# Kernel optimization log

Hardware: AMD Instinct MI355X
Metric: run time of the kernel (lower is better)

Reference implementation:

```python
import jax, jax.numpy as jnp
import numpy as np

B, T, D, H = 64, 512, 256, 512  # batch, seq_len, embed_dim, enc_units


def _lstm(x_tbd, U, xW, reverse):
    """Keras LSTM with activation='sigmoid' (all gates AND candidate/output use sigmoid).
    x_tbd: [T,B,D] (only for shape), xW: precomputed x@W+b [T,B,4H], U: [H,4H].
    Gate order in Keras kernels: i, f, c(g), o."""
    if reverse:
        xW = xW[::-1]
    b = xW.shape[1]
    h0 = jnp.zeros((b, U.shape[0]), xW.dtype)
    c0 = jnp.zeros((b, U.shape[0]), xW.dtype)

    def step(carry, xw):
        h, c = carry
        z = xw + h @ U  # [B,4H]
        i, f, g, o = jnp.split(z, 4, axis=-1)
        i = jax.nn.sigmoid(i)
        f = jax.nn.sigmoid(f)
        g = jax.nn.sigmoid(g)  # activation='sigmoid' (not tanh)
        o = jax.nn.sigmoid(o)
        c_new = f * c + i * g
        h_new = o * jax.nn.sigmoid(c_new)  # activation='sigmoid' (not tanh)
        return (h_new, c_new), h_new

    (h_last, c_last), hs = jax.lax.scan(step, (h0, c0), xW)
    if reverse:
        hs = hs[::-1]  # Bidirectional re-reverses backward outputs to align in time
    return hs, h_last, c_last


def setup_inputs() -> dict:
    key = jax.random.key(0)
    ks = jax.random.split(key, 6)
    s_in = 1.0 / np.sqrt(D)
    s_rec = 1.0 / np.sqrt(H)
    return {
        "x": jax.random.normal(ks[0], (B, T, D), jnp.float32),
        "hidden": jax.random.normal(ks[1], (2 * B, H), jnp.float32),  # unused by call()
        "Wf": jax.random.normal(ks[2], (D, 4 * H), jnp.float32) * s_in,
        "Uf": jax.random.normal(ks[3], (H, 4 * H), jnp.float32) * s_rec,
        "bf": jnp.zeros((4 * H,), jnp.float32),
        "Wb": jax.random.normal(ks[4], (D, 4 * H), jnp.float32) * s_in,
        "Ub": jax.random.normal(ks[5], (H, 4 * H), jnp.float32) * s_rec,
        "bb": jnp.zeros((4 * H,), jnp.float32),
    }


def reference(x, hidden, Wf, Uf, bf, Wb, Ub, bb):
    x_tbd = jnp.transpose(x, (1, 0, 2))  # [T,B,D]
    # Precompute input projections for all timesteps (hoisted out of the scan)
    xWf = jnp.einsum('tbd,dh->tbh', x_tbd, Wf) + bf
    xWb = jnp.einsum('tbd,dh->tbh', x_tbd, Wb) + bb
    hs_f, hF, cF = _lstm(x_tbd, Uf, xWf, reverse=False)
    hs_b, hB, cB = _lstm(x_tbd, Ub, xWb, reverse=True)
    out = 0.5 * (hs_f + hs_b)  # merge_mode='ave'
    out = jnp.transpose(out, (1, 0, 2))  # [B,T,H]
    return out, hF, cF, hB, cB
```

## Files before the change

### kernel.cpp

```cpp
#include <hip/hip_runtime.h>
#include <hip/hip_bf16.h>
#include <cstdint>
#include <cstddef>

#define BB 64
#define TT 512
#define DD 256
#define HH 512
#define G4 2048

typedef __bf16 bf16x8 __attribute__((ext_vector_type(8)));
typedef __bf16 bf16x4 __attribute__((ext_vector_type(4)));
typedef float  f32x4  __attribute__((ext_vector_type(4)));
typedef unsigned long long u64;

__device__ __forceinline__ float sigf(float x) {
  return 1.0f / (1.0f + __expf(-x));
}

__device__ __forceinline__ void drain_vmem() {
  asm volatile("s_waitcnt vmcnt(0)" ::: "memory");
}

__global__ void cvt_x_kernel(const float* __restrict__ x, __bf16* __restrict__ xb) {
  int i = (blockIdx.x * 256 + threadIdx.x) * 4;
  float4 v = *(const float4*)(x + i);
  bf16x4 o;
  o[0] = (__bf16)v.x; o[1] = (__bf16)v.y; o[2] = (__bf16)v.z; o[3] = (__bf16)v.w;
  *(bf16x4*)(xb + i) = o;
}

__launch_bounds__(256, 1)
__global__ void lstm_kernel(const __bf16* __restrict__ xb,
                            const float* __restrict__ Wf, const float* __restrict__ Uf,
                            const float* __restrict__ bf_,
                            const float* __restrict__ Wb, const float* __restrict__ Ub,
                            const float* __restrict__ bb_,
                            __bf16* __restrict__ hbuf,
                            unsigned int* __restrict__ flags,
                            float* __restrict__ out,
                            __bf16* __restrict__ hsb) {
  const int bx  = blockIdx.x;
  const int dir = bx >> 5;
  const int s   = bx & 31;
  const float* Wd = dir ? Wb : Wf;
  const float* Ud = dir ? Ub : Uf;
  const float* bd = dir ? bb_ : bf_;
  unsigned int* flbase = flags + (size_t)dir * 32 * 32;
  unsigned int* myflag = flbase + (size_t)s * 32;
  __bf16* hb = hbuf + (size_t)dir * 2 * BB * HH;

  const int tid  = threadIdx.x;
  const int mt   = tid >> 6;
  const int lane = tid & 63;
  const int j    = lane & 15;
  const int q    = lane >> 4;
  const int colg = s * 16 + j;

  bf16x8 wfrag[4][24];
#pragma unroll
  for (int g = 0; g < 4; ++g) {
    const int col = g * HH + colg;
#pragma unroll
    for (int kt = 0; kt < 24; ++kt) {
      bf16x8 v;
#pragma unroll
      for (int e = 0; e < 8; ++e) {
        const int k = kt * 32 + q * 8 + e;
        const float w = (k < DD) ? Wd[(size_t)k * G4 + col]
                                 : Ud[(size_t)(k - DD) * G4 + col];
        v[e] = (__bf16)w;
      }
      wfrag[g][kt] = v;
    }
  }
  float bg[4];
#pragma unroll
  for (int g = 0; g < 4; ++g) bg[g] = bd[g * HH + colg];

  float cst[4] = {0.f, 0.f, 0.f, 0.f};
  const size_t outTail = (size_t)BB * TT * HH;
  unsigned int* pollp = flbase + (size_t)(lane & 31) * 32;

  for (int tau = 0; tau < TT; ++tau) {
    const int t = dir ? (TT - 1 - tau) : tau;

    const __bf16* xrow = xb + ((size_t)(mt * 16 + j) * TT + t) * DD + q * 8;
    f32x4 acc[4];
#pragma unroll
    for (int g = 0; g < 4; ++g) acc[g] = (f32x4){bg[g], bg[g], bg[g], bg[g]};
#pragma unroll
    for (int kt = 0; kt < 8; ++kt) {
      bf16x8 a = *(const bf16x8*)(xrow + kt * 32);
#pragma unroll
      for (int g = 0; g < 4; ++g)
        acc[g] = __builtin_amdgcn_mfma_f32_16x16x32_bf16(a, wfrag[g][kt], acc[g], 0, 0, 0);
    }

    if (tau) {
      const unsigned int target = (unsigned int)tau;
      for (;;) {
        unsigned int v = __hip_atomic_load(pollp, __ATOMIC_RELAXED, __HIP_MEMORY_SCOPE_AGENT);
        if (__all((int)(v >= target))) break;
        __builtin_amdgcn_s_sleep(8);
      }
      asm volatile("" ::: "memory");
    }

    const u64* hrow = (const u64*)(hb + (size_t)(tau & 1) * (BB * HH)
                                   + (size_t)(mt * 16 + j) * HH) + q * 2;
#pragma unroll
    for (int kt = 0; kt < 16; ++kt) {
      u64 lo = __hip_atomic_load(hrow + kt * 8,     __ATOMIC_RELAXED, __HIP_MEMORY_SCOPE_AGENT);
      u64 hi = __hip_atomic_load(hrow + kt * 8 + 1, __ATOMIC_RELAXED, __HIP_MEMORY_SCOPE_AGENT);
      union { u64 u[2]; bf16x8 v; } tmp;
      tmp.u[0] = lo; tmp.u[1] = hi;
#pragma unroll
      for (int g = 0; g < 4; ++g)
        acc[g] = __builtin_amdgcn_mfma_f32_16x16x32_bf16(tmp.v, wfrag[g][8 + kt], acc[g], 0, 0, 0);
    }

    unsigned int* hnext = (unsigned int*)(hb + (size_t)((tau + 1) & 1) * (BB * HH));
#pragma unroll
    for (int r = 0; r < 4; ++r) {
      const float zi = acc[0][r], zf = acc[1][r], zg = acc[2][r], zo = acc[3][r];
      const float gi = sigf(zi), gf = sigf(zf), gg = sigf(zg), go = sigf(zo);
      const float cn = gf * cst[r] + gi * gg;
      cst[r] = cn;
      const float hn = go * sigf(cn);
      const int orow = mt * 16 + q * 4 + r;

      const unsigned int mine = (unsigned int)__builtin_bit_cast(unsigned short, (__bf16)hn);
      const unsigned int other = (unsigned int)__shfl_xor((int)mine, 1, 64);
      if (!(j & 1)) {
        const unsigned int packed = (other << 16) | mine;
        __hip_atomic_store(hnext + ((size_t)orow * HH + colg) / 2, packed,
                           __ATOMIC_RELAXED, __HIP_MEMORY_SCOPE_AGENT);
      }

      if (dir == 0) {
        __builtin_nontemporal_store(0.5f * hn,
            out + (size_t)orow * (TT * HH) + (size_t)t * HH + colg);
      } else {
        __builtin_nontemporal_store((__bf16)hn,
            hsb + (size_t)t * (BB * HH) + (size_t)orow * HH + colg);
      }
      if (tau == TT - 1) {
        float* base = out + outTail + (size_t)dir * (2 * BB * HH);
        __builtin_nontemporal_store(hn, base + (size_t)orow * HH + colg);
        __builtin_nontemporal_store(cn, base + (size_t)BB * HH + (size_t)orow * HH + colg);
      }
    }

    drain_vmem();
    __syncthreads();
    if (tid == 0)
      __hip_atomic_store(myflag, (unsigned int)(tau + 1), __ATOMIC_RELAXED,
                         __HIP_MEMORY_SCOPE_AGENT);
  }
}

__global__ void combine_kernel(float* __restrict__ out, const __bf16* __restrict__ hsb) {
  const size_t i = ((size_t)blockIdx.x * 256 + threadIdx.x) * 4;
  const size_t b = i >> 18;
  const size_t t = (i >> 9) & 511;
  const size_t c = i & 511;
  bf16x4 hv = *(const bf16x4*)(hsb + t * (BB * HH) + b * HH + c);
  float4 v = *(float4*)(out + i);
  v.x += 0.5f * (float)hv[0];
  v.y += 0.5f * (float)hv[1];
  v.z += 0.5f * (float)hv[2];
  v.w += 0.5f * (float)hv[3];
  *(float4*)(out + i) = v;
}

extern "C" void kernel_launch(void* const* d_in, const int* in_sizes, int n_in,
                              void* d_out, int out_size, void* d_ws, size_t ws_size,
                              hipStream_t stream) {
  (void)in_sizes; (void)n_in; (void)out_size; (void)ws_size;
  const float* x   = (const float*)d_in[0];
  const float* Wf  = (const float*)d_in[2];
  const float* Uf  = (const float*)d_in[3];
  const float* bf_ = (const float*)d_in[4];
  const float* Wb  = (const float*)d_in[5];
  const float* Ub  = (const float*)d_in[6];
  const float* bb_ = (const float*)d_in[7];
  float* out = (float*)d_out;
  char* ws = (char*)d_ws;

  unsigned int* flags = (unsigned int*)ws;
  __bf16* hbuf = (__bf16*)(ws + 8192);
  __bf16* xb   = (__bf16*)(ws + (1 << 19));
  __bf16* hsb  = (__bf16*)(ws + (1 << 19) + (size_t)BB * TT * DD * 2);

  hipMemsetAsync(ws, 0, 1 << 19, stream);
  cvt_x_kernel<<<dim3((BB * TT * DD) / 1024), dim3(256), 0, stream>>>(x, xb);
  lstm_kernel<<<dim3(64), dim3(256), 0, stream>>>(xb, Wf, Uf, bf_, Wb, Ub, bb_,
                                                  hbuf, flags, out, hsb);
  combine_kernel<<<dim3((BB * TT * HH) / 1024), dim3(256), 0, stream>>>(out, hsb);
}
```

Measured before the change: 4.392 ms.

## Split LSTM gate groups across two wave sets with LDS exchange

Doubles the workgroup to 512 threads so each wave computes only two of the four gate matmuls, halving per-wave MFMA chain length and weight registers on the serial recurrent critical path. Gates g and o are passed through shared memory to the waves that do the cell update, which adds an extra barrier per step. Only wave 0 polls the global flags and then releases the other waves through an LDS token, with shorter sleep intervals. The risks are the added barrier and LDS traffic on each timestep, plus the spin-wait on the token.

```diff
diff --git a/kernel.cpp b/kernel.cpp
--- a/kernel.cpp
+++ b/kernel.cpp
@@ -30,7 +30,7 @@
   *(bf16x4*)(xb + i) = o;
 }
 
-__launch_bounds__(256, 1)
+__launch_bounds__(512, 1)
 __global__ void lstm_kernel(const __bf16* __restrict__ xb,
                             const float* __restrict__ Wf, const float* __restrict__ Uf,
                             const float* __restrict__ bf_,
@@ -40,6 +40,9 @@
                             unsigned int* __restrict__ flags,
                             float* __restrict__ out,
                             __bf16* __restrict__ hsb) {
+  __shared__ float zbuf[8 * 4 * 64];
+  __shared__ unsigned int token;
+
   const int bx  = blockIdx.x;
   const int dir = bx >> 5;
   const int s   = bx & 31;
@@ -51,16 +54,20 @@
   __bf16* hb = hbuf + (size_t)dir * 2 * BB * HH;
 
   const int tid  = threadIdx.x;
-  const int mt   = tid >> 6;
+  const int wv   = tid >> 6;
   const int lane = tid & 63;
+  const int mt   = wv & 3;
+  const int gp   = wv >> 2;
   const int j    = lane & 15;
   const int q    = lane >> 4;
   const int colg = s * 16 + j;
 
-  bf16x8 wfrag[4][24];
-#pragma unroll
-  for (int g = 0; g < 4; ++g) {
-    const int col = g * HH + colg;
+  if (tid == 0) token = 0;
+
+  bf16x8 wfrag[2][24];
+#pragma unroll
+  for (int g2 = 0; g2 < 2; ++g2) {
+    const int col = (gp * 2 + g2) * HH + colg;
 #pragma unroll
     for (int kt = 0; kt < 24; ++kt) {
       bf16x8 v;
@@ -71,12 +78,14 @@
                                  : Ud[(size_t)(k - DD) * G4 + col];
         v[e] = (__bf16)w;
       }
-      wfrag[g][kt] = v;
+      wfrag[g2][kt] = v;
     }
   }
-  float bg[4];
-#pragma unroll
-  for (int g = 0; g < 4; ++g) bg[g] = bd[g * HH + colg];
+  float bg2[2];
+#pragma unroll
+  for (int g2 = 0; g2 < 2; ++g2) bg2[g2] = bd[(gp * 2 + g2) * HH + colg];
+
+  __syncthreads();
 
   float cst[4] = {0.f, 0.f, 0.f, 0.f};
   const size_t outTail = (size_t)BB * TT * HH;
@@ -86,23 +95,30 @@
     const int t = dir ? (TT - 1 - tau) : tau;
 
     const __bf16* xrow = xb + ((size_t)(mt * 16 + j) * TT + t) * DD + q * 8;
-    f32x4 acc[4];
-#pragma unroll
-    for (int g = 0; g < 4; ++g) acc[g] = (f32x4){bg[g], bg[g], bg[g], bg[g]};
+    f32x4 acc[2];
+#pragma unroll
+    for (int g2 = 0; g2 < 2; ++g2)
+      acc[g2] = (f32x4){bg2[g2], bg2[g2], bg2[g2], bg2[g2]};
 #pragma unroll
     for (int kt = 0; kt < 8; ++kt) {
       bf16x8 a = *(const bf16x8*)(xrow + kt * 32);
-#pragma unroll
-      for (int g = 0; g < 4; ++g)
-        acc[g] = __builtin_amdgcn_mfma_f32_16x16x32_bf16(a, wfrag[g][kt], acc[g], 0, 0, 0);
+      acc[0] = __builtin_amdgcn_mfma_f32_16x16x32_bf16(a, wfrag[0][kt], acc[0], 0, 0, 0);
+      acc[1] = __builtin_amdgcn_mfma_f32_16x16x32_bf16(a, wfrag[1][kt], acc[1], 0, 0, 0);
     }
 
     if (tau) {
       const unsigned int target = (unsigned int)tau;
-      for (;;) {
-        unsigned int v = __hip_atomic_load(pollp, __ATOMIC_RELAXED, __HIP_MEMORY_SCOPE_AGENT);
-        if (__all((int)(v >= target))) break;
-        __builtin_amdgcn_s_sleep(8);
+      if (wv == 0) {
+        for (;;) {
+          unsigned int v = __hip_atomic_load(pollp, __ATOMIC_RELAXED, __HIP_MEMORY_SCOPE_AGENT);
+          if (__all((int)(v >= target))) break;
+          __builtin_amdgcn_s_sleep(2);
+        }
+        if (lane == 0)
+          __hip_atomic_store(&token, target, __ATOMIC_RELAXED, __HIP_MEMORY_SCOPE_WORKGROUP);
+      } else {
+        while (__hip_atomic_load(&token, __ATOMIC_RELAXED, __HIP_MEMORY_SCOPE_WORKGROUP) < target)
+          __builtin_amdgcn_s_sleep(1);
       }
       asm volatile("" ::: "memory");
     }
@@ -115,44 +131,55 @@
       u64 hi = __hip_atomic_load(hrow + kt * 8 + 1, __ATOMIC_RELAXED, __HIP_MEMORY_SCOPE_AGENT);
       union { u64 u[2]; bf16x8 v; } tmp;
       tmp.u[0] = lo; tmp.u[1] = hi;
-#pragma unroll
-      for (int g = 0; g < 4; ++g)
-        acc[g] = __builtin_amdgcn_mfma_f32_16x16x32_bf16(tmp.v, wfrag[g][8 + kt], acc[g], 0, 0, 0);
-    }
-
-    unsigned int* hnext = (unsigned int*)(hb + (size_t)((tau + 1) & 1) * (BB * HH));
-#pragma unroll
-    for (int r = 0; r < 4; ++r) {
-      const float zi = acc[0][r], zf = acc[1][r], zg = acc[2][r], zo = acc[3][r];
-      const float gi = sigf(zi), gf = sigf(zf), gg = sigf(zg), go = sigf(zo);
-      const float cn = gf * cst[r] + gi * gg;
-      cst[r] = cn;
-      const float hn = go * sigf(cn);
-      const int orow = mt * 16 + q * 4 + r;
-
-      const unsigned int mine = (unsigned int)__builtin_bit_cast(unsigned short, (__bf16)hn);
-      const unsigned int other = (unsigned int)__shfl_xor((int)mine, 1, 64);
-      if (!(j & 1)) {
-        const unsigned int packed = (other << 16) | mine;
-        __hip_atomic_store(hnext + ((size_t)orow * HH + colg) / 2, packed,
-                           __ATOMIC_RELAXED, __HIP_MEMORY_SCOPE_AGENT);
-      }
-
-      if (dir == 0) {
-        __builtin_nontemporal_store(0.5f * hn,
-            out + (size_t)orow * (TT * HH) + (size_t)t * HH + colg);
-      } else {
-        __builtin_nontemporal_store((__bf16)hn,
-            hsb + (size_t)t * (BB * HH) + (size_t)orow * HH + colg);
-      }
-      if (tau == TT - 1) {
-        float* base = out + outTail + (size_t)dir * (2 * BB * HH);
-        __builtin_nontemporal_store(hn, base + (size_t)orow * HH + colg);
-        __builtin_nontemporal_store(cn, base + (size_t)BB * HH + (size_t)orow * HH + colg);
-      }
-    }
-
-    drain_vmem();
+      acc[0] = __builtin_amdgcn_mfma_f32_16x16x32_bf16(tmp.v, wfrag[0][8 + kt], acc[0], 0, 0, 0);
+      acc[1] = __builtin_amdgcn_mfma_f32_16x16x32_bf16(tmp.v, wfrag[1][8 + kt], acc[1], 0, 0, 0);
+    }
+
+    if (gp == 1) {
+#pragma unroll
+      for (int r = 0; r < 4; ++r) {
+        zbuf[((r * 2 + 0) * 4 + mt) * 64 + lane] = acc[0][r];
+        zbuf[((r * 2 + 1) * 4 + mt) * 64 + lane] = acc[1][r];
+      }
+    }
+    __syncthreads();
+
+    if (gp == 0) {
+      unsigned int* hnext = (unsigned int*)(hb + (size_t)((tau + 1) & 1) * (BB * HH));
+#pragma unroll
+      for (int r = 0; r < 4; ++r) {
+        const float zi = acc[0][r], zf = acc[1][r];
+        const float zg = zbuf[((r * 2 + 0) * 4 + mt) * 64 + lane];
+        const float zo = zbuf[((r * 2 + 1) * 4 + mt) * 64 + lane];
+        const float gi = sigf(zi), gf = sigf(zf), gg = sigf(zg), go = sigf(zo);
+        const float cn = gf * cst[r] + gi * gg;
+        cst[r] = cn;
+        const float hn = go * sigf(cn);
+        const int orow = mt * 16 + q * 4 + r;
+
+        const unsigned int mine = (unsigned int)__builtin_bit_cast(unsigned short, (__bf16)hn);
+        const unsigned int other = (unsigned int)__shfl_xor((int)mine, 1, 64);
+        if (!(j & 1)) {
+          const unsigned int packed = (other << 16) | mine;
+          __hip_atomic_store(hnext + ((size_t)orow * HH + colg) / 2, packed,
+                             __ATOMIC_RELAXED, __HIP_MEMORY_SCOPE_AGENT);
+        }
+
+        if (dir == 0) {
+          __builtin_nontemporal_store(0.5f * hn,
+              out + (size_t)orow * (TT * HH) + (size_t)t * HH + colg);
+        } else {
+          __builtin_nontemporal_store((__bf16)hn,
+              hsb + (size_t)t * (BB * HH) + (size_t)orow * HH + colg);
+        }
+        if (tau == TT - 1) {
+          float* base = out + outTail + (size_t)dir * (2 * BB * HH);
+          __builtin_nontemporal_store(hn, base + (size_t)orow * HH + colg);
+          __builtin_nontemporal_store(cn, base + (size_t)BB * HH + (size_t)orow * HH + colg);
+        }
+      }
+      drain_vmem();
+    }
     __syncthreads();
     if (tid == 0)
       __hip_atomic_store(myflag, (unsigned int)(tau + 1), __ATOMIC_RELAXED,
@@ -195,7 +222,7 @@
 
   hipMemsetAsync(ws, 0, 1 << 19, stream);
   cvt_x_kernel<<<dim3((BB * TT * DD) / 1024), dim3(256), 0, stream>>>(x, xb);
-  lstm_kernel<<<dim3(64), dim3(256), 0, stream>>>(xb, Wf, Uf, bf_, Wb, Ub, bb_,
+  lstm_kernel<<<dim3(64), dim3(512), 0, stream>>>(xb, Wf, Uf, bf_, Wb, Ub, bb_,
                                                   hbuf, flags, out, hsb);
   combine_kernel<<<dim3((BB * TT * HH) / 1024), dim3(256), 0, stream>>>(out, hsb);
 }
```

Result: slower. 6.153 ms (+40.1%).
